# Optimization experiments

Measured on AMD Instinct MI355X. Metric: run time of the kernel, lower is better.

The kernel has to match this reference:

```python
import jax, jax.numpy as jnp
import numpy as np

N_NODES = 50000
N_EDGES = 800000


def gcn_conv(x, edge_index, W, b, num_nodes):
    # PyG GCNConv: out = D^-1/2 (A + I) D^-1/2 (X W) + b, with added self-loops.
    xw = x @ W  # [N, F_out]
    src, dst = edge_index[0], edge_index[1]
    loop = jnp.arange(num_nodes, dtype=src.dtype)
    src = jnp.concatenate([src, loop])
    dst = jnp.concatenate([dst, loop])
    # degree (unweighted, after self-loops) on destination nodes
    deg = jax.ops.segment_sum(jnp.ones_like(dst, dtype=xw.dtype), dst,
                              num_segments=num_nodes)
    dinv = jnp.where(deg > 0, jax.lax.rsqrt(deg), 0.0)
    norm = dinv[src] * dinv[dst]  # [E+N]
    msgs = xw[src] * norm[:, None]  # gather + scale
    out = jax.ops.segment_sum(msgs, dst, num_segments=num_nodes)  # scatter-add
    return out + b


def setup_inputs() -> dict:
    key = jax.random.key(0)
    k1, k2, k3, k4 = jax.random.split(key, 4)
    x = jax.random.normal(k1, (N_NODES, 1100), dtype=jnp.float32)
    edge_index = jax.random.randint(k2, (2, N_EDGES), 0, N_NODES, dtype=jnp.int64)
    W1 = jax.random.normal(k3, (512, 256), dtype=jnp.float32) * (1.0 / np.sqrt(512))
    b1 = jnp.zeros((256,), dtype=jnp.float32)
    W2 = jax.random.normal(k4, (256, 128), dtype=jnp.float32) * (1.0 / np.sqrt(256))
    b2 = jnp.zeros((128,), dtype=jnp.float32)
    return {"x": x, "edge_index": edge_index, "W1": W1, "b1": b1,
            "W2": W2, "b2": b2}


def reference(x, edge_index, W1, b1, W2, b2):
    protein_feature = x[:, 588:]  # [N, 512]
    h = gcn_conv(protein_feature, edge_index, W1, b1, N_NODES)
    h = jax.nn.relu(h)
    return gcn_conv(h, edge_index, W2, b2, N_NODES)
```

## Files before the change

### kernel.cpp

```cpp
#include <hip/hip_runtime.h>
#include <hip/hip_bf16.h>
#include <stdint.h>

#define N_NODES 50000
#define N_EDGES 800000

typedef __attribute__((ext_vector_type(8))) __bf16 bf16x8;
typedef __attribute__((ext_vector_type(4))) float floatx4;

__device__ __forceinline__ unsigned short f2bf(float f) {
    union { float f; unsigned u; } v; v.f = f;
    unsigned r = v.u + 0x7fffu + ((v.u >> 16) & 1u);
    return (unsigned short)(r >> 16);
}
__device__ __forceinline__ float bf2f(unsigned short h) {
    union { unsigned u; float f; } v; v.u = ((unsigned)h) << 16;
    return v.f;
}

__global__ __launch_bounds__(256) void count_deg_kernel(
    const int* __restrict__ dst, unsigned* __restrict__ cnt, int nE)
{
    int i = blockIdx.x * blockDim.x + threadIdx.x;
    if (i < nE) {
        unsigned d = (unsigned)dst[i];
        if (d < N_NODES) atomicAdd(&cnt[d], 1u);
    }
}

__global__ __launch_bounds__(256) void dinv_kernel(
    const unsigned* __restrict__ cnt, float* __restrict__ dinv, int n)
{
    int i = blockIdx.x * blockDim.x + threadIdx.x;
    if (i < n) dinv[i] = rsqrtf((float)(cnt[i] + 1u));
}

__global__ __launch_bounds__(256) void block_reduce_kernel(
    const unsigned* __restrict__ cnt, unsigned* __restrict__ blockSums, int n)
{
    __shared__ unsigned s[256];
    int b = blockIdx.x;
    int base = b * 1024;
    unsigned v = 0;
    for (int i = threadIdx.x; i < 1024; i += 256) {
        int idx = base + i;
        v += (idx < n) ? cnt[idx] : 0u;
    }
    s[threadIdx.x] = v; __syncthreads();
    for (int st = 128; st > 0; st >>= 1) {
        if (threadIdx.x < st) s[threadIdx.x] += s[threadIdx.x + st];
        __syncthreads();
    }
    if (threadIdx.x == 0) blockSums[b] = s[0];
}

__global__ __launch_bounds__(64) void scan_sums_kernel(
    unsigned* __restrict__ blockSums, unsigned* __restrict__ off, int nb, int n)
{
    __shared__ unsigned s[64];
    int t = threadIdx.x;
    unsigned v = (t < nb) ? blockSums[t] : 0u;
    s[t] = v; __syncthreads();
    for (int st = 1; st < 64; st <<= 1) {
        unsigned add = (t >= st) ? s[t - st] : 0u;
        __syncthreads();
        s[t] += add;
        __syncthreads();
    }
    if (t < nb) blockSums[t] = s[t] - v;
    if (t == 0) off[n] = s[63];
}

__global__ __launch_bounds__(1024) void block_scan_kernel(
    const unsigned* __restrict__ cnt, const unsigned* __restrict__ blockSums,
    unsigned* __restrict__ off, int n)
{
    __shared__ unsigned s[1024];
    int b = blockIdx.x, t = threadIdx.x;
    int i = b * 1024 + t;
    unsigned v = (i < n) ? cnt[i] : 0u;
    s[t] = v; __syncthreads();
    for (int st = 1; st < 1024; st <<= 1) {
        unsigned add = (t >= st) ? s[t - st] : 0u;
        __syncthreads();
        s[t] += add;
        __syncthreads();
    }
    if (i < n) off[i] = blockSums[b] + s[t] - v;
}

__global__ __launch_bounds__(256) void fill_csr_kernel(
    const int* __restrict__ src, const int* __restrict__ dst,
    const unsigned* __restrict__ off, unsigned* __restrict__ cursor,
    int* __restrict__ csr_src, int nE)
{
    int i = blockIdx.x * blockDim.x + threadIdx.x;
    if (i < nE) {
        unsigned d = (unsigned)dst[i];
        unsigned s = (unsigned)src[i];
        if (d < N_NODES && s < N_NODES) {
            unsigned slot = off[d] + atomicAdd(&cursor[d], 1u);
            csr_src[slot] = (int)s;
        }
    }
}

__global__ __launch_bounds__(256) void split_w_kernel(
    const float* __restrict__ W, unsigned short* __restrict__ Th,
    unsigned short* __restrict__ Tl, int K, int N)
{
    int i = blockIdx.x * blockDim.x + threadIdx.x;
    if (i < K * N) {
        int k = i / N;
        int n = i - k * N;
        float w = W[i];
        unsigned short hi = f2bf(w);
        unsigned short lo = f2bf(w - bf2f(hi));
        Th[(size_t)n * K + k] = hi;
        Tl[(size_t)n * K + k] = lo;
    }
}

#define GBM 128
#define GBN 128
#define GBK 32

__device__ __forceinline__ int chunk_off(int row, int q) {
    return row * 32 + ((q ^ ((row >> 1) & 3)) << 3);
}

template<bool AFP32>
__global__ __launch_bounds__(256) void gemm_mfma_kernel(
    const float* __restrict__ Afp, int lda,
    const unsigned short* __restrict__ Ah, const unsigned short* __restrict__ Al, int apitch,
    const unsigned short* __restrict__ BTh, const unsigned short* __restrict__ BTl,
    const float* __restrict__ dinv, float* __restrict__ Y,
    int M, int K, int N)
{
    __shared__ unsigned short sAh[GBM * GBK];
    __shared__ unsigned short sAl[GBM * GBK];
    __shared__ unsigned short sBh[GBN * GBK];
    __shared__ unsigned short sBl[GBN * GBK];

    const int t    = threadIdx.x;
    const int bm   = blockIdx.x * GBM;
    const int bn   = blockIdx.y * GBN;
    const int w    = t >> 6;
    const int lane = t & 63;
    const int wx   = w & 1;
    const int wy   = w >> 1;
    const int ml   = lane & 15;
    const int quad = lane >> 4;

    const int sr = t >> 1;
    const int q0 = (t & 1) * 2;

    floatx4 zero4 = {0.f, 0.f, 0.f, 0.f};
    floatx4 acc[4][4];
    #pragma unroll
    for (int i = 0; i < 4; ++i)
        #pragma unroll
        for (int j = 0; j < 4; ++j) acc[i][j] = zero4;

    for (int k0 = 0; k0 < K; k0 += GBK) {
        if (AFP32) {
            int gr = bm + sr;
            #pragma unroll
            for (int c = 0; c < 2; ++c) {
                int q = q0 + c;
                float4 v0, v1;
                if (gr < M) {
                    const float* ap = Afp + (size_t)gr * lda + k0 + q * 8;
                    v0 = *(const float4*)(ap);
                    v1 = *(const float4*)(ap + 4);
                } else {
                    v0 = make_float4(0.f,0.f,0.f,0.f);
                    v1 = make_float4(0.f,0.f,0.f,0.f);
                }
                union { unsigned short us[8]; uint4 v; } ph, pl;
                float f[8] = {v0.x, v0.y, v0.z, v0.w, v1.x, v1.y, v1.z, v1.w};
                #pragma unroll
                for (int e = 0; e < 8; ++e) {
                    unsigned short hi = f2bf(f[e]);
                    ph.us[e] = hi;
                    pl.us[e] = f2bf(f[e] - bf2f(hi));
                }
                int off = chunk_off(sr, q);
                *(uint4*)&sAh[off] = ph.v;
                *(uint4*)&sAl[off] = pl.v;
            }
        } else {
            int gr = bm + sr;
            #pragma unroll
            for (int c = 0; c < 2; ++c) {
                int q = q0 + c;
                uint4 vh, vl;
                if (gr < M) {
                    vh = *(const uint4*)(Ah + (size_t)gr * apitch + k0 + q * 8);
                    vl = *(const uint4*)(Al + (size_t)gr * apitch + k0 + q * 8);
                } else {
                    vh = make_uint4(0,0,0,0);
                    vl = make_uint4(0,0,0,0);
                }
                int off = chunk_off(sr, q);
                *(uint4*)&sAh[off] = vh;
                *(uint4*)&sAl[off] = vl;
            }
        }
        {
            int nr = sr;
            const unsigned short* bh = BTh + (size_t)(bn + nr) * K + k0;
            const unsigned short* bl = BTl + (size_t)(bn + nr) * K + k0;
            #pragma unroll
            for (int c = 0; c < 2; ++c) {
                int q = q0 + c;
                uint4 vh = *(const uint4*)(bh + q * 8);
                uint4 vl = *(const uint4*)(bl + q * 8);
                int off = chunk_off(nr, q);
                *(uint4*)&sBh[off] = vh;
                *(uint4*)&sBl[off] = vl;
            }
        }
        __syncthreads();

        bf16x8 fAh[4], fAl[4], fBh[4], fBl[4];
        #pragma unroll
        for (int i = 0; i < 4; ++i) {
            int row = wy * 64 + i * 16 + ml;
            int off = chunk_off(row, quad);
            fAh[i] = *(const bf16x8*)&sAh[off];
            fAl[i] = *(const bf16x8*)&sAl[off];
        }
        #pragma unroll
        for (int j = 0; j < 4; ++j) {
            int nrow = wx * 64 + j * 16 + ml;
            int off = chunk_off(nrow, quad);
            fBh[j] = *(const bf16x8*)&sBh[off];
            fBl[j] = *(const bf16x8*)&sBl[off];
        }

        #pragma unroll
        for (int i = 0; i < 4; ++i)
            #pragma unroll
            for (int j = 0; j < 4; ++j) {
                floatx4 c = acc[i][j];
                c = __builtin_amdgcn_mfma_f32_16x16x32_bf16(fAh[i], fBh[j], c, 0, 0, 0);
                c = __builtin_amdgcn_mfma_f32_16x16x32_bf16(fAl[i], fBh[j], c, 0, 0, 0);
                c = __builtin_amdgcn_mfma_f32_16x16x32_bf16(fAh[i], fBl[j], c, 0, 0, 0);
                acc[i][j] = c;
            }
        __syncthreads();
    }

    #pragma unroll
    for (int i = 0; i < 4; ++i) {
        int rb = bm + wy * 64 + i * 16 + quad * 4;
        float sc[4];
        #pragma unroll
        for (int r = 0; r < 4; ++r) sc[r] = (rb + r < M) ? dinv[rb + r] : 0.f;
        #pragma unroll
        for (int j = 0; j < 4; ++j) {
            int col = bn + wx * 64 + j * 16 + ml;
            #pragma unroll
            for (int r = 0; r < 4; ++r) {
                int grow = rb + r;
                if (grow < M) Y[(size_t)grow * N + col] = acc[i][j][r] * sc[r];
            }
        }
    }
}

__global__ __launch_bounds__(256) void aggregate256_kernel(
    const float* __restrict__ Y, const int* __restrict__ csr_src,
    const unsigned* __restrict__ off, const float* __restrict__ dinv,
    const float* __restrict__ bias,
    unsigned short* __restrict__ Hh, unsigned short* __restrict__ Hl)
{
    const int v  = blockIdx.x * 4 + (threadIdx.x >> 6);
    const int f0 = (threadIdx.x & 63) * 4;

    float4 a0 = *(const float4*)(Y + (size_t)v * 256 + f0);
    float4 a1 = make_float4(0.f,0.f,0.f,0.f);
    float4 a2 = make_float4(0.f,0.f,0.f,0.f);
    float4 a3 = make_float4(0.f,0.f,0.f,0.f);

    const unsigned e0 = off[v], e1 = off[v + 1];
    unsigned j = e0;
    for (; j + 4 <= e1; j += 4) {
        int u0 = csr_src[j + 0];
        int u1 = csr_src[j + 1];
        int u2 = csr_src[j + 2];
        int u3 = csr_src[j + 3];
        float4 m0 = *(const float4*)(Y + (size_t)u0 * 256 + f0);
        float4 m1 = *(const float4*)(Y + (size_t)u1 * 256 + f0);
        float4 m2 = *(const float4*)(Y + (size_t)u2 * 256 + f0);
        float4 m3 = *(const float4*)(Y + (size_t)u3 * 256 + f0);
        a0.x += m0.x; a0.y += m0.y; a0.z += m0.z; a0.w += m0.w;
        a1.x += m1.x; a1.y += m1.y; a1.z += m1.z; a1.w += m1.w;
        a2.x += m2.x; a2.y += m2.y; a2.z += m2.z; a2.w += m2.w;
        a3.x += m3.x; a3.y += m3.y; a3.z += m3.z; a3.w += m3.w;
    }
    for (; j < e1; ++j) {
        float4 m = *(const float4*)(Y + (size_t)csr_src[j] * 256 + f0);
        a0.x += m.x; a0.y += m.y; a0.z += m.z; a0.w += m.w;
    }
    float sx = (a0.x + a1.x) + (a2.x + a3.x);
    float sy = (a0.y + a1.y) + (a2.y + a3.y);
    float sz = (a0.z + a1.z) + (a2.z + a3.z);
    float sw = (a0.w + a1.w) + (a2.w + a3.w);

    float dv = dinv[v];
    float4 b = *(const float4*)(bias + f0);
    float r[4];
    r[0] = fmaxf(sx * dv + b.x, 0.f);
    r[1] = fmaxf(sy * dv + b.y, 0.f);
    r[2] = fmaxf(sz * dv + b.z, 0.f);
    r[3] = fmaxf(sw * dv + b.w, 0.f);

    union { unsigned short us[4]; ushort4 v4; } ph, pl;
    #pragma unroll
    for (int e = 0; e < 4; ++e) {
        unsigned short hi = f2bf(r[e]);
        ph.us[e] = hi;
        pl.us[e] = f2bf(r[e] - bf2f(hi));
    }
    *(ushort4*)(Hh + (size_t)v * 256 + f0) = ph.v4;
    *(ushort4*)(Hl + (size_t)v * 256 + f0) = pl.v4;
}

__global__ __launch_bounds__(256) void aggregate128_kernel(
    const float* __restrict__ Y, const int* __restrict__ csr_src,
    const unsigned* __restrict__ off, const float* __restrict__ dinv,
    const float* __restrict__ bias, float* __restrict__ out)
{
    const int v  = blockIdx.x * 4 + (threadIdx.x >> 6);
    const int f0 = (threadIdx.x & 63) * 2;

    float2 a0 = *(const float2*)(Y + (size_t)v * 128 + f0);
    float2 a1 = make_float2(0.f,0.f);
    float2 a2 = make_float2(0.f,0.f);
    float2 a3 = make_float2(0.f,0.f);

    const unsigned e0 = off[v], e1 = off[v + 1];
    unsigned j = e0;
    for (; j + 4 <= e1; j += 4) {
        int u0 = csr_src[j + 0];
        int u1 = csr_src[j + 1];
        int u2 = csr_src[j + 2];
        int u3 = csr_src[j + 3];
        float2 m0 = *(const float2*)(Y + (size_t)u0 * 128 + f0);
        float2 m1 = *(const float2*)(Y + (size_t)u1 * 128 + f0);
        float2 m2 = *(const float2*)(Y + (size_t)u2 * 128 + f0);
        float2 m3 = *(const float2*)(Y + (size_t)u3 * 128 + f0);
        a0.x += m0.x; a0.y += m0.y;
        a1.x += m1.x; a1.y += m1.y;
        a2.x += m2.x; a2.y += m2.y;
        a3.x += m3.x; a3.y += m3.y;
    }
    for (; j < e1; ++j) {
        float2 m = *(const float2*)(Y + (size_t)csr_src[j] * 128 + f0);
        a0.x += m.x; a0.y += m.y;
    }
    float sx = (a0.x + a1.x) + (a2.x + a3.x);
    float sy = (a0.y + a1.y) + (a2.y + a3.y);

    float dv = dinv[v];
    float2 b = *(const float2*)(bias + f0);
    float2 r = make_float2(sx * dv + b.x, sy * dv + b.y);
    *(float2*)(out + (size_t)v * 128 + f0) = r;
}

extern "C" void kernel_launch(void* const* d_in, const int* in_sizes, int n_in,
                              void* d_out, int out_size, void* d_ws, size_t ws_size,
                              hipStream_t stream)
{
    const float* x  = (const float*)d_in[0];
    const int*   ei = (const int*)d_in[1];
    const float* W1 = (const float*)d_in[2];
    const float* b1 = (const float*)d_in[3];
    const float* W2 = (const float*)d_in[4];
    const float* b2 = (const float*)d_in[5];
    float*       out = (float*)d_out;

    const int* e_src = ei;
    const int* e_dst = ei + N_EDGES;

    char* ws = (char*)d_ws;
    size_t o = 0;
    auto carve = [&](size_t bytes) -> char* {
        char* p = ws + o;
        o = (o + bytes + 511) & ~(size_t)511;
        return p;
    };
    unsigned*       cnt    = (unsigned*)carve((size_t)N_NODES * 4);
    unsigned*       cursor = (unsigned*)carve((size_t)N_NODES * 4);
    unsigned*       off    = (unsigned*)carve((size_t)(N_NODES + 1) * 4);
    unsigned*       bsums  = (unsigned*)carve(64 * 4);
    float*          dinv   = (float*)carve((size_t)N_NODES * 4);
    int*            csr    = (int*)carve((size_t)N_EDGES * 4);
    unsigned short* WT1h   = (unsigned short*)carve((size_t)512 * 256 * 2);
    unsigned short* WT1l   = (unsigned short*)carve((size_t)512 * 256 * 2);
    unsigned short* WT2h   = (unsigned short*)carve((size_t)256 * 128 * 2);
    unsigned short* WT2l   = (unsigned short*)carve((size_t)256 * 128 * 2);
    float*          y      = (float*)carve((size_t)N_NODES * 256 * 4);
    unsigned short* Hh     = (unsigned short*)carve((size_t)N_NODES * 256 * 2);
    unsigned short* Hl     = (unsigned short*)carve((size_t)N_NODES * 256 * 2);
    (void)ws_size;

    hipMemsetAsync(cnt,    0, (size_t)N_NODES * 4, stream);
    hipMemsetAsync(cursor, 0, (size_t)N_NODES * 4, stream);

    const int nScanBlocks = (N_NODES + 1023) / 1024;

    count_deg_kernel<<<(N_EDGES + 255) / 256, 256, 0, stream>>>(e_dst, cnt, N_EDGES);
    dinv_kernel<<<(N_NODES + 255) / 256, 256, 0, stream>>>(cnt, dinv, N_NODES);
    block_reduce_kernel<<<nScanBlocks, 256, 0, stream>>>(cnt, bsums, N_NODES);
    scan_sums_kernel<<<1, 64, 0, stream>>>(bsums, off, nScanBlocks, N_NODES);
    block_scan_kernel<<<nScanBlocks, 1024, 0, stream>>>(cnt, bsums, off, N_NODES);
    fill_csr_kernel<<<(N_EDGES + 255) / 256, 256, 0, stream>>>(e_src, e_dst, off, cursor, csr, N_EDGES);

    split_w_kernel<<<(512 * 256 + 255) / 256, 256, 0, stream>>>(W1, WT1h, WT1l, 512, 256);
    split_w_kernel<<<(256 * 128 + 255) / 256, 256, 0, stream>>>(W2, WT2h, WT2l, 256, 128);

    {
        dim3 grid((N_NODES + GBM - 1) / GBM, 256 / GBN);
        gemm_mfma_kernel<true><<<grid, 256, 0, stream>>>(
            x + 588, 1100, nullptr, nullptr, 0, WT1h, WT1l, dinv, y,
            N_NODES, 512, 256);
    }
    aggregate256_kernel<<<N_NODES / 4, 256, 0, stream>>>(y, csr, off, dinv, b1, Hh, Hl);

    {
        dim3 grid((N_NODES + GBM - 1) / GBM, 128 / GBN);
        gemm_mfma_kernel<false><<<grid, 256, 0, stream>>>(
            nullptr, 0, Hh, Hl, 256, WT2h, WT2l, dinv, y,
            N_NODES, 256, 128);
    }
    aggregate128_kernel<<<N_NODES / 4, 256, 0, stream>>>(y, csr, off, dinv, b2, out);
}
```

Before: 658.6 us.

## Widen first GEMM tile to full N and vectorize second aggregation

The first-layer GEMM now uses a 128x256 tile so each block covers all 256 output columns. The fp32 strided x slice is then read and split into bf16 hi/lo once instead of twice across two column blocks. The B-fragment loads are interleaved into the MFMA loop, and launch bounds ask for two blocks per CU. The 128-wide aggregation moves from float2 with 64 lanes per node to float4 with 32 lanes per node, giving wider gathers and more nodes per block. The doubled accumulator count (4x8 floatx4 per wave) raises register pressure and may cut occupancy or cause spills.

```diff
diff --git a/kernel.cpp b/kernel.cpp
--- a/kernel.cpp
+++ b/kernel.cpp
@@ -122,29 +122,31 @@
 }
 
 #define GBM 128
-#define GBN 128
 #define GBK 32
 
 __device__ __forceinline__ int chunk_off(int row, int q) {
     return row * 32 + ((q ^ ((row >> 1) & 3)) << 3);
 }
 
-template<bool AFP32>
-__global__ __launch_bounds__(256) void gemm_mfma_kernel(
+template<bool AFP32, int BN>
+__global__ __launch_bounds__(256, 2) void gemm_mfma_kernel(
     const float* __restrict__ Afp, int lda,
     const unsigned short* __restrict__ Ah, const unsigned short* __restrict__ Al, int apitch,
     const unsigned short* __restrict__ BTh, const unsigned short* __restrict__ BTl,
     const float* __restrict__ dinv, float* __restrict__ Y,
     int M, int K, int N)
 {
+    constexpr int WCOLS = BN / 2;
+    constexpr int NJ    = WCOLS / 16;
+
     __shared__ unsigned short sAh[GBM * GBK];
     __shared__ unsigned short sAl[GBM * GBK];
-    __shared__ unsigned short sBh[GBN * GBK];
-    __shared__ unsigned short sBl[GBN * GBK];
+    __shared__ unsigned short sBh[BN * GBK];
+    __shared__ unsigned short sBl[BN * GBK];
 
     const int t    = threadIdx.x;
     const int bm   = blockIdx.x * GBM;
-    const int bn   = blockIdx.y * GBN;
+    const int bn   = blockIdx.y * BN;
     const int w    = t >> 6;
     const int lane = t & 63;
     const int wx   = w & 1;
@@ -156,11 +158,11 @@
     const int q0 = (t & 1) * 2;
 
     floatx4 zero4 = {0.f, 0.f, 0.f, 0.f};
-    floatx4 acc[4][4];
+    floatx4 acc[4][NJ];
     #pragma unroll
     for (int i = 0; i < 4; ++i)
         #pragma unroll
-        for (int j = 0; j < 4; ++j) acc[i][j] = zero4;
+        for (int j = 0; j < NJ; ++j) acc[i][j] = zero4;
 
     for (int k0 = 0; k0 < K; k0 += GBK) {
         if (AFP32) {
@@ -207,8 +209,9 @@
                 *(uint4*)&sAl[off] = vl;
             }
         }
-        {
-            int nr = sr;
+        #pragma unroll
+        for (int r = 0; r < BN / 128; ++r) {
+            int nr = sr + r * 128;
             const unsigned short* bh = BTh + (size_t)(bn + nr) * K + k0;
             const unsigned short* bl = BTl + (size_t)(bn + nr) * K + k0;
             #pragma unroll
@@ -223,7 +226,7 @@
         }
         __syncthreads();
 
-        bf16x8 fAh[4], fAl[4], fBh[4], fBl[4];
+        bf16x8 fAh[4], fAl[4];
         #pragma unroll
         for (int i = 0; i < 4; ++i) {
             int row = wy * 64 + i * 16 + ml;
@@ -231,24 +234,22 @@
             fAh[i] = *(const bf16x8*)&sAh[off];
             fAl[i] = *(const bf16x8*)&sAl[off];
         }
-        #pragma unroll
-        for (int j = 0; j < 4; ++j) {
-            int nrow = wx * 64 + j * 16 + ml;
+
+        #pragma unroll
+        for (int j = 0; j < NJ; ++j) {
+            int nrow = wx * WCOLS + j * 16 + ml;
             int off = chunk_off(nrow, quad);
-            fBh[j] = *(const bf16x8*)&sBh[off];
-            fBl[j] = *(const bf16x8*)&sBl[off];
-        }
-
-        #pragma unroll
-        for (int i = 0; i < 4; ++i)
+            bf16x8 fBh = *(const bf16x8*)&sBh[off];
+            bf16x8 fBl = *(const bf16x8*)&sBl[off];
             #pragma unroll
-            for (int j = 0; j < 4; ++j) {
+            for (int i = 0; i < 4; ++i) {
                 floatx4 c = acc[i][j];
-                c = __builtin_amdgcn_mfma_f32_16x16x32_bf16(fAh[i], fBh[j], c, 0, 0, 0);
-                c = __builtin_amdgcn_mfma_f32_16x16x32_bf16(fAl[i], fBh[j], c, 0, 0, 0);
-                c = __builtin_amdgcn_mfma_f32_16x16x32_bf16(fAh[i], fBl[j], c, 0, 0, 0);
+                c = __builtin_amdgcn_mfma_f32_16x16x32_bf16(fAh[i], fBh, c, 0, 0, 0);
+                c = __builtin_amdgcn_mfma_f32_16x16x32_bf16(fAl[i], fBh, c, 0, 0, 0);
+                c = __builtin_amdgcn_mfma_f32_16x16x32_bf16(fAh[i], fBl, c, 0, 0, 0);
                 acc[i][j] = c;
             }
+        }
         __syncthreads();
     }
 
@@ -259,8 +260,8 @@
         #pragma unroll
         for (int r = 0; r < 4; ++r) sc[r] = (rb + r < M) ? dinv[rb + r] : 0.f;
         #pragma unroll
-        for (int j = 0; j < 4; ++j) {
-            int col = bn + wx * 64 + j * 16 + ml;
+        for (int j = 0; j < NJ; ++j) {
+            int col = bn + wx * WCOLS + j * 16 + ml;
             #pragma unroll
             for (int r = 0; r < 4; ++r) {
                 int grow = rb + r;
@@ -333,13 +334,13 @@
     const unsigned* __restrict__ off, const float* __restrict__ dinv,
     const float* __restrict__ bias, float* __restrict__ out)
 {
-    const int v  = blockIdx.x * 4 + (threadIdx.x >> 6);
-    const int f0 = (threadIdx.x & 63) * 2;
-
-    float2 a0 = *(const float2*)(Y + (size_t)v * 128 + f0);
-    float2 a1 = make_float2(0.f,0.f);
-    float2 a2 = make_float2(0.f,0.f);
-    float2 a3 = make_float2(0.f,0.f);
+    const int v  = blockIdx.x * 8 + (threadIdx.x >> 5);
+    const int f0 = (threadIdx.x & 31) * 4;
+
+    float4 a0 = *(const float4*)(Y + (size_t)v * 128 + f0);
+    float4 a1 = make_float4(0.f,0.f,0.f,0.f);
+    float4 a2 = make_float4(0.f,0.f,0.f,0.f);
+    float4 a3 = make_float4(0.f,0.f,0.f,0.f);
 
     const unsigned e0 = off[v], e1 = off[v + 1];
     unsigned j = e0;
@@ -348,26 +349,32 @@
         int u1 = csr_src[j + 1];
         int u2 = csr_src[j + 2];
         int u3 = csr_src[j + 3];
-        float2 m0 = *(const float2*)(Y + (size_t)u0 * 128 + f0);
-        float2 m1 = *(const float2*)(Y + (size_t)u1 * 128 + f0);
-        float2 m2 = *(const float2*)(Y + (size_t)u2 * 128 + f0);
-        float2 m3 = *(const float2*)(Y + (size_t)u3 * 128 + f0);
-        a0.x += m0.x; a0.y += m0.y;
-        a1.x += m1.x; a1.y += m1.y;
-        a2.x += m2.x; a2.y += m2.y;
-        a3.x += m3.x; a3.y += m3.y;
+        float4 m0 = *(const float4*)(Y + (size_t)u0 * 128 + f0);
+        float4 m1 = *(const float4*)(Y + (size_t)u1 * 128 + f0);
+        float4 m2 = *(const float4*)(Y + (size_t)u2 * 128 + f0);
+        float4 m3 = *(const float4*)(Y + (size_t)u3 * 128 + f0);
+        a0.x += m0.x; a0.y += m0.y; a0.z += m0.z; a0.w += m0.w;
+        a1.x += m1.x; a1.y += m1.y; a1.z += m1.z; a1.w += m1.w;
+        a2.x += m2.x; a2.y += m2.y; a2.z += m2.z; a2.w += m2.w;
+        a3.x += m3.x; a3.y += m3.y; a3.z += m3.z; a3.w += m3.w;
     }
     for (; j < e1; ++j) {
-        float2 m = *(const float2*)(Y + (size_t)csr_src[j] * 128 + f0);
-        a0.x += m.x; a0.y += m.y;
+        float4 m = *(const float4*)(Y + (size_t)csr_src[j] * 128 + f0);
+        a0.x += m.x; a0.y += m.y; a0.z += m.z; a0.w += m.w;
     }
     float sx = (a0.x + a1.x) + (a2.x + a3.x);
     float sy = (a0.y + a1.y) + (a2.y + a3.y);
+    float sz = (a0.z + a1.z) + (a2.z + a3.z);
+    float sw = (a0.w + a1.w) + (a2.w + a3.w);
 
     float dv = dinv[v];
-    float2 b = *(const float2*)(bias + f0);
-    float2 r = make_float2(sx * dv + b.x, sy * dv + b.y);
-    *(float2*)(out + (size_t)v * 128 + f0) = r;
+    float4 b = *(const float4*)(bias + f0);
+    float4 r;
+    r.x = sx * dv + b.x;
+    r.y = sy * dv + b.y;
+    r.z = sz * dv + b.z;
+    r.w = sw * dv + b.w;
+    *(float4*)(out + (size_t)v * 128 + f0) = r;
 }
 
 extern "C" void kernel_launch(void* const* d_in, const int* in_sizes, int n_in,
@@ -423,18 +430,18 @@
     split_w_kernel<<<(256 * 128 + 255) / 256, 256, 0, stream>>>(W2, WT2h, WT2l, 256, 128);
 
     {
-        dim3 grid((N_NODES + GBM - 1) / GBM, 256 / GBN);
-        gemm_mfma_kernel<true><<<grid, 256, 0, stream>>>(
+        dim3 grid((N_NODES + GBM - 1) / GBM, 1);
+        gemm_mfma_kernel<true, 256><<<grid, 256, 0, stream>>>(
             x + 588, 1100, nullptr, nullptr, 0, WT1h, WT1l, dinv, y,
             N_NODES, 512, 256);
     }
     aggregate256_kernel<<<N_NODES / 4, 256, 0, stream>>>(y, csr, off, dinv, b1, Hh, Hl);
 
     {
-        dim3 grid((N_NODES + GBM - 1) / GBM, 128 / GBN);
-        gemm_mfma_kernel<false><<<grid, 256, 0, stream>>>(
+        dim3 grid((N_NODES + GBM - 1) / GBM, 1);
+        gemm_mfma_kernel<false, 128><<<grid, 256, 0, stream>>>(
             nullptr, 0, Hh, Hl, 256, WT2h, WT2l, dinv, y,
             N_NODES, 256, 128);
     }
-    aggregate128_kernel<<<N_NODES / 4, 256, 0, stream>>>(y, csr, off, dinv, b2, out);
-}
+    aggregate128_kernel<<<N_NODES / 8, 256, 0, stream>>>(y, csr, off, dinv, b2, out);
+}
```

After: 646.9 us. Within noise of the previous version (-1.8%).
